# Performance work log

Hardware: AMD Instinct MI355X
Metric: run time of the kernel (lower is better)

## Reference

```python
import jax, jax.numpy as jnp
import numpy as np
from jax import lax

V_VOX, T_PTS, D, H, W = 12000, 35, 10, 200, 176
EPS = 1e-5


def _bn(x, g, b, axes, shape):
    m = x.mean(axes, keepdims=True)
    v = x.var(axes, keepdims=True)  # biased var, matches torch BN training stats
    return g.reshape(shape) * (x - m) * lax.rsqrt(v + EPS) + b.reshape(shape)


def _conv3d(x, w, b):
    y = lax.conv_general_dilated(x, w, (1, 1, 1), 'SAME',
                                 dimension_numbers=('NCDHW', 'OIDHW', 'NCDHW'))
    return y + b[None, :, None, None, None]


def _conv2d(x, w, b):
    y = lax.conv_general_dilated(x, w, (1, 1), 'SAME',
                                 dimension_numbers=('NCHW', 'OIHW', 'NCHW'))
    return y + b[None, :, None, None]


def setup_inputs() -> dict:
    key = jax.random.key(0)
    ks = jax.random.split(key, 12)
    voxels = jax.random.normal(ks[0], (1, V_VOX, T_PTS, 4), jnp.float32)
    # unique voxel coordinates (the torch loop overwrites on duplicates; unique avoids ambiguity)
    rng = np.random.default_rng(0)
    flat = rng.choice(D * H * W, size=V_VOX, replace=False)
    z = flat // (H * W); rem = flat % (H * W)
    coords = jnp.asarray(np.stack([z, rem // W, rem % W], axis=1), dtype=jnp.int32)
    s = 0.05
    p = dict(
        w_lin=jax.random.normal(ks[1], (32, 4), jnp.float32) * s,
        b_lin=jnp.zeros((32,), jnp.float32),
        g_bn0=jnp.ones((32,), jnp.float32), be_bn0=jnp.zeros((32,), jnp.float32),
        w_c3a=jax.random.normal(ks[2], (64, 32, 3, 3, 3), jnp.float32) * s,
        b_c3a=jnp.zeros((64,), jnp.float32),
        g_bn1=jnp.ones((64,), jnp.float32), be_bn1=jnp.zeros((64,), jnp.float32),
        w_c3b=jax.random.normal(ks[3], (64, 64, 3, 3, 3), jnp.float32) * s,
        b_c3b=jnp.zeros((64,), jnp.float32),
        g_bn2=jnp.ones((64,), jnp.float32), be_bn2=jnp.zeros((64,), jnp.float32),
        w_r1=jax.random.normal(ks[4], (128, 64, 3, 3), jnp.float32) * s,
        b_r1=jnp.zeros((128,), jnp.float32),
        w_r2=jax.random.normal(ks[5], (8, 128, 1, 1), jnp.float32) * s,
        b_r2=jnp.zeros((8,), jnp.float32),
    )
    return dict(voxels=voxels, coords=coords, **p)


def reference(voxels, coords, w_lin, b_lin, g_bn0, be_bn0,
              w_c3a, b_c3a, g_bn1, be_bn1, w_c3b, b_c3b, g_bn2, be_bn2,
              w_r1, b_r1, w_r2, b_r2):
    B, V, T, C = voxels.shape
    # SimpleVFE: linear -> BN1d (batch stats) -> relu -> max over points
    h = voxels.reshape(B * V * T, C) @ w_lin.T + b_lin          # [BVT,32]
    h = jax.nn.relu(_bn(h, g_bn0, be_bn0, 0, (1, 32)))
    feats = h.reshape(B, V, T, 32).max(axis=2)                  # [B,V,32]
    # fused scatter into dense volume (replaces per-voxel python loop)
    volume = jnp.zeros((B, 32, D, H, W), voxels.dtype)
    volume = volume.at[0, :, coords[:, 0], coords[:, 1], coords[:, 2]].set(feats[0])
    # 3D backbone
    x = jax.nn.relu(_bn(_conv3d(volume, w_c3a, b_c3a), g_bn1, be_bn1, (0, 2, 3, 4), (1, 64, 1, 1, 1)))
    x = jax.nn.relu(_bn(_conv3d(x, w_c3b, b_c3b), g_bn2, be_bn2, (0, 2, 3, 4), (1, 64, 1, 1, 1)))
    x = x.mean(axis=2)                                          # collapse depth -> [B,64,H,W]
    # RPN head
    out = _conv2d(jax.nn.relu(_conv2d(x, w_r1, b_r1)), w_r2, b_r2)  # [B,8,H,W]
    box = jnp.concatenate([out[:, 0:3], jnp.exp(out[:, 3:6]),
                           jnp.tanh(out[:, 6:7]), jax.nn.sigmoid(out[:, 7:8])], axis=1)
    return box
```

## Files before the change

kernel.cpp:

```cpp
#include <hip/hip_runtime.h>
#include <math.h>

#define V_VOX 12000
#define T_PTS 35
#define DD 10
#define HH 200
#define WW 176
#define EPSV 1e-5f

#define DP 12
#define HP 202
#define WP 178
#define PPLN (HP * WP)
#define PVOX (DP * PPLN)
#define NPIX (DD * HH * WW)
#define HWPIX (HH * WW)

typedef _Float16 half_t;
typedef _Float16 f16x8 __attribute__((ext_vector_type(8)));
typedef float f32x4 __attribute__((ext_vector_type(4)));

#define WPA_OFF 0
#define WPB_OFF 110592
#define WPR1_OFF 331776
#define STATS_OFF 479232
#define VOLP_OFF 2019328
#define X1P_OFF 29633536
#define Y_OFF 84861952
#define PLANE_OFF 129917952
#define R1OUT_OFF 134520320

#define S_BN0S 0
#define S_BN0Q 32
#define S_BN1S 64
#define S_BN1Q 128
#define S_BN2S 192
#define S_BN2Q 256

__device__ __forceinline__ void gload16(const half_t* g, half_t* l) {
    __builtin_amdgcn_global_load_lds(
        (const __attribute__((address_space(1))) void*)g,
        (__attribute__((address_space(3))) void*)l, 16, 0, 0);
}

__device__ __forceinline__ void pack1(const float* __restrict__ w, half_t* __restrict__ wp,
                                      int IC, int NT, int OC, int id) {
    int OCT = OC >> 4, KH = IC >> 5;
    int j = id & 7;
    int lane = (id >> 3) & 63;
    int rest = id >> 9;
    int ot = rest % OCT; rest /= OCT;
    int kh = rest % KH;
    int tap = rest / KH;
    int oc = ot * 16 + (lane & 15);
    int ic = kh * 32 + (lane >> 4) * 8 + j;
    wp[id] = (half_t)w[(oc * IC + ic) * NT + tap];
}

__global__ void k_pack_all(const float* __restrict__ wA, const float* __restrict__ wB,
                           const float* __restrict__ wR1, half_t* __restrict__ wpA,
                           half_t* __restrict__ wpB, half_t* __restrict__ wpR1) {
    int id = blockIdx.x * 256 + threadIdx.x;
    if (id < 55296) pack1(wA, wpA, 32, 27, 64, id);
    else if (id < 165888) pack1(wB, wpB, 64, 27, 64, id - 55296);
    else if (id < 239616) pack1(wR1, wpR1, 64, 9, 128, id - 165888);
}

__global__ void k_vfe_stats(const float4* __restrict__ vox, const float* __restrict__ w_lin,
                            const float* __restrict__ b_lin, float* __restrict__ S) {
    int tid = blockIdx.x * 256 + threadIdx.x;
    int c = threadIdx.x & 31;
    float4 w = ((const float4*)w_lin)[c];
    float bl = b_lin[c];
    float s = 0.f, q = 0.f;
    const int np = V_VOX * T_PTS;
    int stride = gridDim.x * 8;
    for (int p = tid >> 5; p < np; p += stride) {
        float4 v = vox[p];
        float d = v.x * w.x + v.y * w.y + v.z * w.z + v.w * w.w + bl;
        s += d;
        q += d * d;
    }
    s += __shfl_xor(s, 32);
    q += __shfl_xor(q, 32);
    if ((threadIdx.x & 63) < 32) {
        atomicAdd(&S[S_BN0S + c], s);
        atomicAdd(&S[S_BN0Q + c], q);
    }
}

__global__ void k_vfe_max(const float4* __restrict__ vox, const float* __restrict__ w_lin,
                          const float* __restrict__ b_lin, const float* __restrict__ S,
                          const float* __restrict__ g, const float* __restrict__ be,
                          const int* __restrict__ coords, half_t* __restrict__ volp) {
    __shared__ float lA[32], lB[32];
    if (threadIdx.x < 32) {
        int c = threadIdx.x;
        float m = S[S_BN0S + c] * (1.f / 420000.f);
        float v = S[S_BN0Q + c] * (1.f / 420000.f) - m * m;
        float a = g[c] * rsqrtf(v + EPSV);
        lA[c] = a;
        lB[c] = be[c] - m * a;
    }
    __syncthreads();
    int id = blockIdx.x * 256 + threadIdx.x;
    if (id >= V_VOX * 32) return;
    int c = id & 31;
    int v = id >> 5;
    float4 w = ((const float4*)w_lin)[c];
    float bl = b_lin[c], A = lA[c], B = lB[c];
    float m = 0.f;
    for (int t = 0; t < T_PTS; t++) {
        float4 p = vox[v * T_PTS + t];
        float d = p.x * w.x + p.y * w.y + p.z * w.z + p.w * w.w + bl;
        m = fmaxf(m, A * d + B);
    }
    int z = coords[v * 3 + 0];
    int y = coords[v * 3 + 1];
    int x = coords[v * 3 + 2];
    volp[(((z + 1) * HP + (y + 1)) * WP + (x + 1)) * 32 + c] = (half_t)m;
}

template <int KH, int DZ, int OCTP, int NWG, bool RELU, bool STATS>
__global__ __launch_bounds__(256, 4) void k_conv(const half_t* __restrict__ in,
                                                 size_t khstride,
                                                 const half_t* __restrict__ wp,
                                                 const float* __restrict__ bias,
                                                 half_t* __restrict__ out,
                                                 float* __restrict__ ssum,
                                                 float* __restrict__ ssq) {
    constexpr int OC = OCTP * 16;
    constexpr int NS = DZ * KH;
    __shared__ __align__(16) half_t tA[21 * 512];
    __shared__ __align__(16) half_t tB[18 * 512];

    const int tid = threadIdx.x;
    const int lane = tid & 63;
    const int wv = tid >> 6;

    constexpr int qc = NWG >> 3, rc = NWG & 7;
    int hw = blockIdx.x;
    int xcd = hw & 7, idx = hw >> 3;
    int work = (xcd < rc ? xcd * (qc + 1) : rc * (qc + 1) + (xcd - rc) * qc) + idx;
    int ocb, z0, x0, y0b;
    if (DZ == 3) {
        ocb = (work & 1) * 2;
        int t = work >> 1;
        x0 = (t % 11) * 16; t /= 11;
        y0b = (t % 13) * 16;
        z0 = t / 13;
    } else {
        ocb = (work & 3) * 2;
        int t = work >> 2;
        x0 = (t % 11) * 16;
        y0b = (t / 11) * 16;
        z0 = 0;
    }
    const int y0w = y0b + wv * 4;
    const bool valid = (y0w < HH);
    const int colc = lane & 15, grp = lane >> 4;

    unsigned gofsA[6];
#pragma unroll
    for (int i = 0; i < 6; ++i) {
        int run = wv + 4 * i;
        int c = run * 64 + lane;
        if (c > 1295) c = 1295;
        int pixhi = c >> 3, s = c & 7;
        int b = ((s >> 2) ^ (pixhi >> 1)) & 1;
        int q = ((s ^ b) & 1) | ((((s >> 1) ^ pixhi) & 1) << 1);
        int pix = pixhi * 2 + b;
        int row = pix / 18, px = pix - row * 18;
        int srow = y0b + row;
        if (srow > HP - 1) srow = HP - 1;
        gofsA[i] = (unsigned)((srow * WP + x0 + px) * 32 + q * 8);
    }

    f32x4 acc[4][2];
#pragma unroll
    for (int m = 0; m < 4; m++)
#pragma unroll
        for (int n = 0; n < 2; n++) acc[m][n] = (f32x4)(0.f);

#pragma unroll 1
    for (int s = 0; s < NS; ++s) {
        const int dz = s / KH, kh = s % KH;
        const half_t* sl = in + (size_t)kh * khstride
                           + (size_t)(z0 + dz) * (DZ == 3 ? (size_t)PPLN * 32 : 0);
#pragma unroll
        for (int i = 0; i < 6; ++i) {
            int run = wv + 4 * i;
            if (run < 21) gload16(sl + gofsA[i], &tA[run * 512]);
        }
#pragma unroll
        for (int i = 0; i < 5; ++i) {
            int r = wv + 4 * i;
            if (r < 18) {
                int tap = r >> 1, hf = r & 1;
                const half_t* g = wp + (((size_t)(dz * 9 + tap) * KH + kh) * OCTP + ocb + hf) * 512
                                  + lane * 8;
                gload16(g, &tB[r * 512]);
            }
        }
        asm volatile("s_waitcnt vmcnt(0)" ::: "memory");
        __syncthreads();

        if (valid) {
#pragma unroll
            for (int dx = 0; dx < 3; ++dx) {
                f16x8 Af[6];
#pragma unroll
                for (int r = 0; r < 6; ++r) {
                    int pix = (wv * 4 + r) * 18 + colc + dx;
                    int ah = ((pix << 5) | (grp << 3)) ^ ((pix & 7) << 3);
                    Af[r] = *(const f16x8*)&tA[ah];
                }
#pragma unroll
                for (int dy = 0; dy < 3; ++dy) {
                    f16x8 Bf[2];
#pragma unroll
                    for (int n = 0; n < 2; ++n)
                        Bf[n] = *(const f16x8*)&tB[((dy * 3 + dx) * 2 + n) * 512 + lane * 8];
#pragma unroll
                    for (int m = 0; m < 4; ++m)
#pragma unroll
                        for (int n = 0; n < 2; ++n)
                            acc[m][n] = __builtin_amdgcn_mfma_f32_16x16x32_f16(
                                Af[dy + m], Bf[n], acc[m][n], 0, 0, 0);
                }
            }
        }
        __syncthreads();
    }

    if (!valid) return;
#pragma unroll
    for (int n = 0; n < 2; ++n) {
        int oc = (ocb + n) * 16 + colc;
        float bv = bias[oc];
        float s = 0.f, q = 0.f;
#pragma unroll
        for (int m = 0; m < 4; ++m) {
            int yy = y0w + m;
#pragma unroll
            for (int i = 0; i < 4; ++i) {
                int xx = x0 + grp * 4 + i;
                float v = acc[m][n][i] + bv;
                if (STATS) { s += v; q += v * v; }
                float w = RELU ? fmaxf(v, 0.f) : v;
                out[((size_t)(z0 * HH + yy) * WW + xx) * OC + oc] = (half_t)w;
            }
        }
        if (STATS) {
            s += __shfl_xor(s, 16); s += __shfl_xor(s, 32);
            q += __shfl_xor(q, 16); q += __shfl_xor(q, 32);
            if (lane < 16) {
                atomicAdd(&ssum[oc], s);
                atomicAdd(&ssq[oc], q);
            }
        }
    }
}

__global__ void k_activate(const half_t* __restrict__ y1, const float* __restrict__ S,
                           const float* __restrict__ g, const float* __restrict__ be,
                           half_t* __restrict__ xp) {
    __shared__ float lA[64], lB[64];
    if (threadIdx.x < 64) {
        int c = threadIdx.x;
        float m = S[S_BN1S + c] * (1.f / 352000.f);
        float v = S[S_BN1Q + c] * (1.f / 352000.f) - m * m;
        float a = g[c] * rsqrtf(v + EPSV);
        lA[c] = a;
        lB[c] = be[c] - m * a;
    }
    __syncthreads();
    int id = blockIdx.x * 256 + threadIdx.x;
    if (id >= PVOX * 8) return;
    int c0 = (id & 7) * 8;
    int pix = id >> 3;
    int zp = pix / PPLN;
    int rem = pix - zp * PPLN;
    int yp = rem / WP;
    int xq = rem - yp * WP;
    f16x8 o;
    if (zp >= 1 && zp <= DD && yp >= 1 && yp <= HH && xq >= 1 && xq <= WW) {
        size_t p = ((size_t)((zp - 1) * HH + (yp - 1)) * WW + (xq - 1));
        f16x8 v = *(const f16x8*)(y1 + p * 64 + c0);
#pragma unroll
        for (int j = 0; j < 8; j++)
            o[j] = (half_t)fmaxf(lA[c0 + j] * (float)v[j] + lB[c0 + j], 0.f);
    } else {
#pragma unroll
        for (int j = 0; j < 8; j++) o[j] = (half_t)0.f;
    }
    int khp = c0 >> 5;
    *(f16x8*)(xp + (size_t)khp * PVOX * 32 + (size_t)pix * 32 + (c0 & 31)) = o;
}

__global__ void k_depthmean(const half_t* __restrict__ y2, const float* __restrict__ S,
                            const float* __restrict__ g, const float* __restrict__ be,
                            half_t* __restrict__ plane) {
    __shared__ float lA[64], lB[64];
    if (threadIdx.x < 64) {
        int c = threadIdx.x;
        float m = S[S_BN2S + c] * (1.f / 352000.f);
        float v = S[S_BN2Q + c] * (1.f / 352000.f) - m * m;
        float a = g[c] * rsqrtf(v + EPSV);
        lA[c] = a;
        lB[c] = be[c] - m * a;
    }
    __syncthreads();
    int id = blockIdx.x * 256 + threadIdx.x;
    if (id >= PPLN * 8) return;
    int c8 = id & 7;
    int pix = id >> 3;
    int yp = pix / WP;
    int xq = pix - yp * WP;
    f16x8 o;
    if (yp >= 1 && yp <= HH && xq >= 1 && xq <= WW) {
        float A[8], B[8], sacc[8];
#pragma unroll
        for (int j = 0; j < 8; j++) {
            A[j] = lA[c8 * 8 + j];
            B[j] = lB[c8 * 8 + j];
            sacc[j] = 0.f;
        }
        const half_t* base = y2 + ((size_t)(yp - 1) * WW + (xq - 1)) * 64 + c8 * 8;
#pragma unroll
        for (int z = 0; z < DD; z++) {
            f16x8 v = *(const f16x8*)(base + (size_t)z * HWPIX * 64);
#pragma unroll
            for (int j = 0; j < 8; j++)
                sacc[j] += fmaxf(A[j] * (float)v[j] + B[j], 0.f);
        }
#pragma unroll
        for (int j = 0; j < 8; j++) o[j] = (half_t)(sacc[j] * 0.1f);
    } else {
#pragma unroll
        for (int j = 0; j < 8; j++) o[j] = (half_t)0.f;
    }
    int khp = c8 >> 2;
    *(f16x8*)(plane + (size_t)khp * PPLN * 32 + (size_t)pix * 32 + (c8 & 3) * 8) = o;
}

__global__ void k_r2(const half_t* __restrict__ r1o, const float* __restrict__ w,
                     const float* __restrict__ bias, float* __restrict__ outp) {
    __shared__ float wsm[1024];
    for (int i = threadIdx.x; i < 1024; i += 256) wsm[i] = w[i];
    __syncthreads();
    int p = blockIdx.x * 256 + threadIdx.x;
    if (p >= HWPIX) return;
    float acc[8];
#pragma unroll
    for (int o = 0; o < 8; o++) acc[o] = bias[o];
    const half_t* rb = r1o + (size_t)p * 128;
#pragma unroll 4
    for (int icb = 0; icb < 128; icb += 8) {
        f16x8 v = *(const f16x8*)(rb + icb);
#pragma unroll
        for (int j = 0; j < 8; j++) {
            float vv = (float)v[j];
#pragma unroll
            for (int o = 0; o < 8; o++) acc[o] += vv * wsm[o * 128 + icb + j];
        }
    }
    outp[0 * HWPIX + p] = acc[0];
    outp[1 * HWPIX + p] = acc[1];
    outp[2 * HWPIX + p] = acc[2];
    outp[3 * HWPIX + p] = expf(acc[3]);
    outp[4 * HWPIX + p] = expf(acc[4]);
    outp[5 * HWPIX + p] = expf(acc[5]);
    outp[6 * HWPIX + p] = tanhf(acc[6]);
    outp[7 * HWPIX + p] = 1.f / (1.f + expf(-acc[7]));
}

extern "C" void kernel_launch(void* const* d_in, const int* in_sizes, int n_in,
                              void* d_out, int out_size, void* d_ws, size_t ws_size,
                              hipStream_t stream) {
    const float4* voxels = (const float4*)d_in[0];
    const int* coords = (const int*)d_in[1];
    const float* w_lin = (const float*)d_in[2];
    const float* b_lin = (const float*)d_in[3];
    const float* g_bn0 = (const float*)d_in[4];
    const float* be_bn0 = (const float*)d_in[5];
    const float* w_c3a = (const float*)d_in[6];
    const float* b_c3a = (const float*)d_in[7];
    const float* g_bn1 = (const float*)d_in[8];
    const float* be_bn1 = (const float*)d_in[9];
    const float* w_c3b = (const float*)d_in[10];
    const float* b_c3b = (const float*)d_in[11];
    const float* g_bn2 = (const float*)d_in[12];
    const float* be_bn2 = (const float*)d_in[13];
    const float* w_r1 = (const float*)d_in[14];
    const float* b_r1 = (const float*)d_in[15];
    const float* w_r2 = (const float*)d_in[16];
    const float* b_r2 = (const float*)d_in[17];

    char* ws = (char*)d_ws;
    half_t* wpA = (half_t*)(ws + WPA_OFF);
    half_t* wpB = (half_t*)(ws + WPB_OFF);
    half_t* wpR1 = (half_t*)(ws + WPR1_OFF);
    float* S = (float*)(ws + STATS_OFF);
    half_t* volp = (half_t*)(ws + VOLP_OFF);
    half_t* x1p = (half_t*)(ws + X1P_OFF);
    half_t* Y = (half_t*)(ws + Y_OFF);
    half_t* plane = (half_t*)(ws + PLANE_OFF);
    half_t* r1out = (half_t*)(ws + R1OUT_OFF);
    float* outp = (float*)d_out;

    hipMemsetAsync(S, 0, 320 * sizeof(float), stream);
    hipMemsetAsync(volp, 0, (size_t)PVOX * 32 * sizeof(half_t), stream);

    k_pack_all<<<936, 256, 0, stream>>>(w_c3a, w_c3b, w_r1, wpA, wpB, wpR1);

    k_vfe_stats<<<512, 256, 0, stream>>>(voxels, w_lin, b_lin, S);
    k_vfe_max<<<1500, 256, 0, stream>>>(voxels, w_lin, b_lin, S, g_bn0, be_bn0,
                                        coords, volp);

    k_conv<1, 3, 4, 2860, false, true><<<2860, 256, 0, stream>>>(
        volp, 0, wpA, b_c3a, Y, S + S_BN1S, S + S_BN1Q);
    k_activate<<<13484, 256, 0, stream>>>(Y, S, g_bn1, be_bn1, x1p);

    k_conv<2, 3, 4, 2860, false, true><<<2860, 256, 0, stream>>>(
        x1p, (size_t)PVOX * 32, wpB, b_c3b, Y, S + S_BN2S, S + S_BN2Q);

    k_depthmean<<<1124, 256, 0, stream>>>(Y, S, g_bn2, be_bn2, plane);

    k_conv<2, 1, 8, 572, true, false><<<572, 256, 0, stream>>>(
        plane, (size_t)PPLN * 32, wpR1, b_r1, r1out, nullptr, nullptr);
    k_r2<<<138, 256, 0, stream>>>(r1out, w_r2, b_r2, outp);
}
```

Measured before the change: 446.1 us.

## Warp-specialize conv kernel with producer waves and double-buffered LDS

The implicit-GEMM conv kernel gains two dedicated producer waves that stream the next input and weight tiles into a second LDS buffer. Meanwhile the four consumer waves run MFMAs on the current buffer, and one barrier per stage replaces the earlier load-wait-compute-sync sequence. The aim is to hide global-to-LDS load latency behind the matrix math. In exchange, LDS use per block doubles and the block grows to 384 threads, which likely cuts resident blocks per CU and the number of compute waves available to hide latency.

```diff
diff --git a/kernel.cpp b/kernel.cpp
--- a/kernel.cpp
+++ b/kernel.cpp
@@ -122,7 +122,7 @@
 }
 
 template <int KH, int DZ, int OCTP, int NWG, bool RELU, bool STATS>
-__global__ __launch_bounds__(256, 4) void k_conv(const half_t* __restrict__ in,
+__global__ __launch_bounds__(384, 3) void k_conv(const half_t* __restrict__ in,
                                                  size_t khstride,
                                                  const half_t* __restrict__ wp,
                                                  const float* __restrict__ bias,
@@ -131,12 +131,13 @@
                                                  float* __restrict__ ssq) {
     constexpr int OC = OCTP * 16;
     constexpr int NS = DZ * KH;
-    __shared__ __align__(16) half_t tA[21 * 512];
-    __shared__ __align__(16) half_t tB[18 * 512];
+    __shared__ __align__(16) half_t tA[2][21 * 512];
+    __shared__ __align__(16) half_t tB[2][18 * 512];
 
     const int tid = threadIdx.x;
     const int lane = tid & 63;
     const int wv = tid >> 6;
+    const bool producer = (wv >= 4);
 
     constexpr int qc = NWG >> 3, rc = NWG & 7;
     int hw = blockIdx.x;
@@ -157,23 +158,27 @@
         z0 = 0;
     }
     const int y0w = y0b + wv * 4;
-    const bool valid = (y0w < HH);
+    const bool valid = (!producer) && (y0w < HH);
     const int colc = lane & 15, grp = lane >> 4;
 
-    unsigned gofsA[6];
-#pragma unroll
-    for (int i = 0; i < 6; ++i) {
-        int run = wv + 4 * i;
-        int c = run * 64 + lane;
-        if (c > 1295) c = 1295;
-        int pixhi = c >> 3, s = c & 7;
-        int b = ((s >> 2) ^ (pixhi >> 1)) & 1;
-        int q = ((s ^ b) & 1) | ((((s >> 1) ^ pixhi) & 1) << 1);
-        int pix = pixhi * 2 + b;
-        int row = pix / 18, px = pix - row * 18;
-        int srow = y0b + row;
-        if (srow > HP - 1) srow = HP - 1;
-        gofsA[i] = (unsigned)((srow * WP + x0 + px) * 32 + q * 8);
+    const int pw = wv - 4;
+    unsigned gofsA[11];
+    if (producer) {
+#pragma unroll
+        for (int i = 0; i < 11; ++i) {
+            int run = pw * 11 + i;
+            if (run > 20) run = 20;
+            int c = run * 64 + lane;
+            if (c > 1295) c = 1295;
+            int pixhi = c >> 3, s = c & 7;
+            int b = ((s >> 2) ^ (pixhi >> 1)) & 1;
+            int q = ((s ^ b) & 1) | ((((s >> 1) ^ pixhi) & 1) << 1);
+            int pix = pixhi * 2 + b;
+            int row = pix / 18, px = pix - row * 18;
+            int srow = y0b + row;
+            if (srow > HP - 1) srow = HP - 1;
+            gofsA[i] = (unsigned)((srow * WP + x0 + px) * 32 + q * 8);
+        }
     }
 
     f32x4 acc[4][2];
@@ -182,30 +187,38 @@
 #pragma unroll
         for (int n = 0; n < 2; n++) acc[m][n] = (f32x4)(0.f);
 
-#pragma unroll 1
-    for (int s = 0; s < NS; ++s) {
+    auto STAGE = [&](int s, int buf) {
         const int dz = s / KH, kh = s % KH;
         const half_t* sl = in + (size_t)kh * khstride
                            + (size_t)(z0 + dz) * (DZ == 3 ? (size_t)PPLN * 32 : 0);
 #pragma unroll
-        for (int i = 0; i < 6; ++i) {
-            int run = wv + 4 * i;
-            if (run < 21) gload16(sl + gofsA[i], &tA[run * 512]);
-        }
-#pragma unroll
-        for (int i = 0; i < 5; ++i) {
-            int r = wv + 4 * i;
-            if (r < 18) {
-                int tap = r >> 1, hf = r & 1;
-                const half_t* g = wp + (((size_t)(dz * 9 + tap) * KH + kh) * OCTP + ocb + hf) * 512
-                                  + lane * 8;
-                gload16(g, &tB[r * 512]);
-            }
-        }
+        for (int i = 0; i < 11; ++i) {
+            int run = pw * 11 + i;
+            if (run < 21) gload16(sl + gofsA[i], &tA[buf][run * 512]);
+        }
+#pragma unroll
+        for (int i = 0; i < 9; ++i) {
+            int r = pw * 9 + i;
+            int tap = r >> 1, hf = r & 1;
+            const half_t* g = wp + (((size_t)(dz * 9 + tap) * KH + kh) * OCTP + ocb + hf) * 512
+                              + lane * 8;
+            gload16(g, &tB[buf][r * 512]);
+        }
+    };
+
+    if (producer) {
+        STAGE(0, 0);
         asm volatile("s_waitcnt vmcnt(0)" ::: "memory");
-        __syncthreads();
-
-        if (valid) {
+    }
+    __builtin_amdgcn_s_barrier();
+
+#pragma unroll 1
+    for (int s = 0; s < NS; ++s) {
+        if (producer) {
+            if (s + 1 < NS) STAGE(s + 1, (s + 1) & 1);
+            asm volatile("s_waitcnt vmcnt(0)" ::: "memory");
+        } else if (valid) {
+            const int buf = s & 1;
 #pragma unroll
             for (int dx = 0; dx < 3; ++dx) {
                 f16x8 Af[6];
@@ -213,14 +226,14 @@
                 for (int r = 0; r < 6; ++r) {
                     int pix = (wv * 4 + r) * 18 + colc + dx;
                     int ah = ((pix << 5) | (grp << 3)) ^ ((pix & 7) << 3);
-                    Af[r] = *(const f16x8*)&tA[ah];
+                    Af[r] = *(const f16x8*)&tA[buf][ah];
                 }
 #pragma unroll
                 for (int dy = 0; dy < 3; ++dy) {
                     f16x8 Bf[2];
 #pragma unroll
                     for (int n = 0; n < 2; ++n)
-                        Bf[n] = *(const f16x8*)&tB[((dy * 3 + dx) * 2 + n) * 512 + lane * 8];
+                        Bf[n] = *(const f16x8*)&tB[buf][((dy * 3 + dx) * 2 + n) * 512 + lane * 8];
 #pragma unroll
                     for (int m = 0; m < 4; ++m)
 #pragma unroll
@@ -229,8 +242,9 @@
                                 Af[dy + m], Bf[n], acc[m][n], 0, 0, 0);
                 }
             }
-        }
-        __syncthreads();
+            asm volatile("s_waitcnt lgkmcnt(0)" ::: "memory");
+        }
+        __builtin_amdgcn_s_barrier();
     }
 
     if (!valid) return;
@@ -418,16 +432,16 @@
     k_vfe_max<<<1500, 256, 0, stream>>>(voxels, w_lin, b_lin, S, g_bn0, be_bn0,
                                         coords, volp);
 
-    k_conv<1, 3, 4, 2860, false, true><<<2860, 256, 0, stream>>>(
+    k_conv<1, 3, 4, 2860, false, true><<<2860, 384, 0, stream>>>(
         volp, 0, wpA, b_c3a, Y, S + S_BN1S, S + S_BN1Q);
     k_activate<<<13484, 256, 0, stream>>>(Y, S, g_bn1, be_bn1, x1p);
 
-    k_conv<2, 3, 4, 2860, false, true><<<2860, 256, 0, stream>>>(
+    k_conv<2, 3, 4, 2860, false, true><<<2860, 384, 0, stream>>>(
         x1p, (size_t)PVOX * 32, wpB, b_c3b, Y, S + S_BN2S, S + S_BN2Q);
 
     k_depthmean<<<1124, 256, 0, stream>>>(Y, S, g_bn2, be_bn2, plane);
 
-    k_conv<2, 1, 8, 572, true, false><<<572, 256, 0, stream>>>(
+    k_conv<2, 1, 8, 572, true, false><<<572, 384, 0, stream>>>(
         plane, (size_t)PPLN * 32, wpR1, b_r1, r1out, nullptr, nullptr);
     k_r2<<<138, 256, 0, stream>>>(r1out, w_r2, b_r2, outp);
 }
```

New measurement: 459.3 us. 3.0% more time.
